# Optimization experiments

Hardware: AMD Instinct MI355X
Metric: run time of the kernel (lower is better)

Reference implementation:

```python
import jax, jax.numpy as jnp
import numpy as np
from jax import lax

BATCH = 512
FS = 24        # filter_size
QDIM = 11      # sort-of-clevr question vector length
IMG = 80       # 80 -> 40 -> 20 -> 10 -> 5 via four stride-2 convs
D = 5
OBJ = D * D    # 25 objects
PAIR_IN = (FS + 2) * 2 + QDIM  # 63
HID = 256
EPS = 1e-5


def setup_inputs() -> dict:
    key = jax.random.key(0)
    ks = jax.random.split(key, 24)

    def n(k, shape, s=0.05):
        return jax.random.normal(k, shape, jnp.float32) * s

    inp = {
        "img": jax.random.normal(ks[0], (BATCH, 3, IMG, IMG), jnp.float32),
        "qst": jax.random.normal(ks[1], (QDIM, BATCH), jnp.float32),
    }
    chans = [3, FS, FS, FS]
    ki = 2
    for l in range(4):
        inp[f"cw{l+1}"] = n(ks[ki], (FS, chans[l], 3, 3)); ki += 1
        inp[f"cb{l+1}"] = jnp.zeros((FS,), jnp.float32)
        inp[f"bg{l+1}"] = jnp.ones((FS,), jnp.float32)
        inp[f"bb{l+1}"] = jnp.zeros((FS,), jnp.float32)
    g_in = [PAIR_IN, HID, HID, HID]
    for l in range(4):
        inp[f"g{l+1}w"] = n(ks[ki], (HID, g_in[l])); ki += 1
        inp[f"g{l+1}b"] = jnp.zeros((HID,), jnp.float32)
    inp["f1w"] = n(ks[ki], (HID, HID)); ki += 1
    inp["f1b"] = jnp.zeros((HID,), jnp.float32)
    inp["fc2w"] = n(ks[ki], (HID, HID)); ki += 1
    inp["fc2b"] = jnp.zeros((HID,), jnp.float32)
    inp["fc3w"] = n(ks[ki], (10, HID)); ki += 1
    inp["fc3b"] = jnp.zeros((10,), jnp.float32)
    return inp


def _conv_bn(x, w, b, gamma, beta):
    # conv stride 2, pad 1 -> relu -> batchnorm (training-mode batch stats)
    y = lax.conv_general_dilated(x, w, (2, 2), [(1, 1), (1, 1)],
                                 dimension_numbers=("NCHW", "OIHW", "NCHW"))
    y = jax.nn.relu(y + b[None, :, None, None])
    mean = y.mean(axis=(0, 2, 3))
    var = y.var(axis=(0, 2, 3))
    inv = gamma * lax.rsqrt(var + EPS)
    return (y - mean[None, :, None, None]) * inv[None, :, None, None] + beta[None, :, None, None]


def _lin(x, w, b):
    return x @ w.T + b


def reference(img, qst,
              cw1, cb1, bg1, bb1, cw2, cb2, bg2, bb2,
              cw3, cb3, bg3, bb3, cw4, cb4, bg4, bb4,
              g1w, g1b, g2w, g2b, g3w, g3b, g4w, g4b,
              f1w, f1b, fc2w, fc2b, fc3w, fc3b):
    q = qst.T  # [mb, QDIM] (torch.transpose(qst,0,1).float())

    x = _conv_bn(img, cw1, cb1, bg1, bb1)
    x = _conv_bn(x, cw2, cb2, bg2, bb2)
    x = _conv_bn(x, cw3, cb3, bg3, bb3)
    x = _conv_bn(x, cw4, cb4, bg4, bb4)   # [mb, FS, 5, 5]

    mb = x.shape[0]
    x_flat = x.reshape(mb, FS, OBJ).transpose(0, 2, 1)  # [mb, 25, FS]

    idx = jnp.arange(OBJ)
    coord = jnp.stack([(idx // 5 - 2) / 2.0, (idx % 5 - 2) / 2.0], axis=-1).astype(jnp.float32)
    x_flat = jnp.concatenate([x_flat, jnp.broadcast_to(coord, (mb, OBJ, 2))], axis=2)  # [mb,25,FS+2]

    # pair[b, k, i] = concat(obj_i, obj_k, q)  (matches torch x_i/x_j/cat layout)
    oi = jnp.broadcast_to(x_flat[:, None, :, :], (mb, OBJ, OBJ, FS + 2))
    oj = jnp.broadcast_to(x_flat[:, :, None, :], (mb, OBJ, OBJ, FS + 2))
    qq = jnp.broadcast_to(q[:, None, None, :], (mb, OBJ, OBJ, QDIM))
    pairs = jnp.concatenate([oi, oj, qq], axis=3).reshape(mb * OBJ * OBJ, PAIR_IN)

    h = jax.nn.relu(_lin(pairs, g1w, g1b))
    h = jax.nn.relu(_lin(h, g2w, g2b))
    h = jax.nn.relu(_lin(h, g3w, g3b))
    h = jax.nn.relu(_lin(h, g4w, g4b))
    x_g = h.reshape(mb, OBJ * OBJ, HID).sum(axis=1)  # [mb, 256]

    x_f = jax.nn.relu(_lin(x_g, f1w, f1b))
    x_f = jax.nn.relu(_lin(x_f, fc2w, fc2b))
    # dropout treated as identity (eval-mode deterministic reference)
    logits = _lin(x_f, fc3w, fc3b)
    return jax.nn.log_softmax(logits, axis=-1)
```

## Files before the change

### kernel.cpp

```cpp
#include <hip/hip_runtime.h>
#include <math.h>

#define MB    512
#define FS    24
#define QDIM  11
#define OBJ   25
#define HID   256

typedef unsigned short u16;
typedef __attribute__((ext_vector_type(8))) __bf16 bf16x8;
typedef __attribute__((ext_vector_type(4))) __bf16 bf16x4;
typedef __attribute__((ext_vector_type(4))) float f32x4;
typedef __attribute__((ext_vector_type(8))) float f32x8;

__device__ __forceinline__ float bf2f(u16 h) {
    return __uint_as_float(((unsigned int)h) << 16);
}
__device__ __forceinline__ u16 f2bf(float f) {
    unsigned int u = __float_as_uint(f);
    return (u16)((u + 0x7FFFu + ((u >> 16) & 1u)) >> 16);
}

__global__ __launch_bounds__(256) void prep_all(
    const float* __restrict__ g2w, const float* __restrict__ g3w,
    const float* __restrict__ g4w, u16* __restrict__ wfrag,
    const float* __restrict__ cw1, const float* __restrict__ cw2,
    const float* __restrict__ cw3, const float* __restrict__ cw4,
    float* __restrict__ wt1, u16* __restrict__ wcfrag)
{
    if (blockIdx.x < 768) {
        int idx = blockIdx.x * 256 + threadIdx.x;
        int jj = idx & 7;
        int lane = (idx >> 3) & 63;
        int tn = (idx >> 9) & 15;
        int c = (idx >> 13) & 7;
        int l = idx >> 16;
        const float* W = (l == 0) ? g2w : ((l == 1) ? g3w : g4w);
        int n = tn * 16 + (lane & 15);
        int k = c * 32 + (lane >> 4) * 8 + jj;
        wfrag[idx] = f2bf(W[n * 256 + k]);
    } else {
        int idx = (blockIdx.x - 768) * 256 + threadIdx.x;
        if (idx < 648) {
            int k = idx / 24, oc = idx % 24;
            wt1[idx] = cw1[oc * 27 + k];
        } else if (idx < 648 + 27648) {
            int t = idx - 648;
            int l = t / 9216, r = t % 9216;
            int cell = r / 1024, rr = r % 1024;
            int o = rr / 512, q = rr % 512;
            int lane = q / 8, j = q % 8;
            int oc = o * 16 + (lane & 15);
            int ic = (lane >> 4) * 8 + j;
            const float* w = (l == 0) ? cw2 : ((l == 1) ? cw3 : cw4);
            u16 v = 0;
            if (oc < 24 && ic < 24) v = f2bf(w[oc * 216 + ic * 9 + cell]);
            wcfrag[t] = v;
        }
    }
}

__global__ __launch_bounds__(256) void conv1_t(
    const float* __restrict__ img, const float* __restrict__ wt1,
    const float* __restrict__ bias, float* __restrict__ yout,
    float* __restrict__ stats)
{
    __shared__ float tile[3 * 21 * 85];
    __shared__ float wS[648];
    __shared__ float part[48];
    const int tid = threadIdx.x;
    const int b   = blockIdx.x >> 2;
    const int y0  = (blockIdx.x & 3) * 10;
    const int iy_base = 2 * y0 - 1;
    for (int e = tid; e < 648; e += 256) wS[e] = wt1[e];
    for (int e = tid; e < 3 * 21 * 85; e += 256) {
        int ixt = e % 85; int rem = e / 85;
        int iyl = rem % 21; int ic = rem / 21;
        int iy = iy_base + iyl, ix = ixt - 1;
        float v = 0.f;
        if ((unsigned)iy < 80u && (unsigned)ix < 80u)
            v = img[((size_t)(b * 3 + ic) * 80 + iy) * 80 + ix];
        tile[e] = v;
    }
    if (tid < 48) part[tid] = 0.f;
    __syncthreads();

    float rsum[24], rsq[24];
#pragma unroll
    for (int oc = 0; oc < 24; oc++) { rsum[oc] = 0.f; rsq[oc] = 0.f; }

#pragma unroll 1
    for (int pp = 0; pp < 2; pp++) {
        const int pxl = tid + pp * 256;
        const bool active = pxl < 400;
        const int pxc = active ? pxl : 0;
        const int yl = pxc / 40, x = pxc % 40;
        float acc[24];
#pragma unroll
        for (int oc = 0; oc < 24; oc++) acc[oc] = bias[oc];
#pragma unroll 1
        for (int ic = 0; ic < 3; ic++) {
#pragma unroll 1
            for (int ky = 0; ky < 3; ky++) {
#pragma unroll 1
                for (int kx = 0; kx < 3; kx++) {
                    const int k = (ic * 3 + ky) * 3 + kx;
                    float xin = tile[ic * 1785 + (2 * yl + ky) * 85 + (2 * x + kx)];
                    const float4* wrow = (const float4*)&wS[k * 24];
#pragma unroll
                    for (int g = 0; g < 6; g++) {
                        float4 wv = wrow[g];
                        acc[g * 4 + 0] = fmaf(xin, wv.x, acc[g * 4 + 0]);
                        acc[g * 4 + 1] = fmaf(xin, wv.y, acc[g * 4 + 1]);
                        acc[g * 4 + 2] = fmaf(xin, wv.z, acc[g * 4 + 2]);
                        acc[g * 4 + 3] = fmaf(xin, wv.w, acc[g * 4 + 3]);
                    }
                }
            }
        }
#pragma unroll
        for (int oc = 0; oc < 24; oc++)
            acc[oc] = active ? fmaxf(acc[oc], 0.f) : 0.f;
        if (active) {
            float* op = &yout[((size_t)b * 1600 + (y0 + yl) * 40 + x) * 24];
#pragma unroll
            for (int g = 0; g < 6; g++)
                *(float4*)&op[g * 4] = make_float4(acc[g * 4], acc[g * 4 + 1],
                                                   acc[g * 4 + 2], acc[g * 4 + 3]);
        }
#pragma unroll
        for (int oc = 0; oc < 24; oc++) {
            rsum[oc] += acc[oc];
            rsq[oc]  += acc[oc] * acc[oc];
        }
    }

    {
        float v[48];
#pragma unroll
        for (int oc = 0; oc < 24; oc++) { v[oc] = rsum[oc]; v[24 + oc] = rsq[oc]; }
        const int ln = tid & 63;
#pragma unroll
        for (int i = 0; i < 48; i++) v[i] += __shfl_xor(v[i], 1, 64);
        {
            const bool bs = (ln & 1) != 0;
#pragma unroll
            for (int i = 0; i < 24; i++) v[i] = bs ? v[24 + i] : v[i];
        }
#pragma unroll
        for (int i = 0; i < 24; i++) v[i] += __shfl_xor(v[i], 2, 64);
        {
            const bool bs = (ln & 2) != 0;
#pragma unroll
            for (int i = 0; i < 12; i++) v[i] = bs ? v[12 + i] : v[i];
        }
#pragma unroll
        for (int i = 0; i < 12; i++) v[i] += __shfl_xor(v[i], 4, 64);
        {
            const bool bs = (ln & 4) != 0;
#pragma unroll
            for (int i = 0; i < 6; i++) v[i] = bs ? v[6 + i] : v[i];
        }
#pragma unroll
        for (int i = 0; i < 6; i++) v[i] += __shfl_xor(v[i], 8, 64);
        {
            const bool bs = (ln & 8) != 0;
#pragma unroll
            for (int i = 0; i < 3; i++) v[i] = bs ? v[3 + i] : v[i];
        }
#pragma unroll
        for (int i = 0; i < 3; i++) {
            v[i] += __shfl_xor(v[i], 16, 64);
            v[i] += __shfl_xor(v[i], 32, 64);
        }
        if (ln < 16) {
            const int base = (ln & 1) * 24 + ((ln >> 1) & 1) * 12
                           + ((ln >> 2) & 1) * 6 + ((ln >> 3) & 1) * 3;
#pragma unroll
            for (int i = 0; i < 3; i++) atomicAdd(&part[base + i], v[i]);
        }
    }
    __syncthreads();
    if (tid < 48) atomicAdd(&stats[tid], part[tid]);
}

template<int HIN, int HOUT, int YT, int MT>
__global__ __launch_bounds__(256) void convM(
    const float* __restrict__ yin,
    const float* __restrict__ stp, const float* __restrict__ gam,
    const float* __restrict__ bet, float invN,
    const u16* __restrict__ wcf_g,
    const float* __restrict__ bias,
    float* __restrict__ yout, float* __restrict__ stats)
{
    constexpr int ROWS = 2 * YT + 1;
    constexpr int R    = 2 * HOUT + 1;
    constexpr int POS  = ROWS * R;
    constexpr int NPX  = HOUT * HOUT;
    constexpr int NPXB = YT * HOUT;
    constexpr int TILES = HOUT / YT;
    constexpr int MTPW = (MT + 3) / 4;
    __shared__ __align__(16) u16 tile[POS * 24 + 16];
    __shared__ float scW[48];
    __shared__ float part[48];
    const int tid  = threadIdx.x;
    const int b    = (TILES == 1) ? blockIdx.x : (int)(blockIdx.x / TILES);
    const int y0   = (TILES == 1) ? 0 : (int)(blockIdx.x % TILES) * YT;
    const int lane = tid & 63, wave = tid >> 6;
    const int r16  = lane & 15, quad = lane >> 4;

    if (tid < 24) {
        float m   = stp[tid] * invN;
        float var = stp[24 + tid] * invN - m * m;
        float inv = gam[tid] * rsqrtf(var + 1e-5f);
        scW[tid]      = inv;
        scW[24 + tid] = bet[tid] - m * inv;
    }
    if (tid < 48) part[tid] = 0.f;

    bf16x8 wcf[9][2];
#pragma unroll
    for (int c = 0; c < 9; c++)
#pragma unroll
        for (int o = 0; o < 2; o++)
            wcf[c][o] = *(const bf16x8*)&wcf_g[((c * 2 + o) * 64 + lane) * 8];

    __syncthreads();

    f32x8 scv[3], ofv[3];
#pragma unroll
    for (int g = 0; g < 3; g++)
#pragma unroll
        for (int c2 = 0; c2 < 8; c2++) {
            scv[g][c2] = scW[g * 8 + c2];
            ofv[g][c2] = scW[24 + g * 8 + c2];
        }

    const int iy_base = 2 * y0 - 1;
    for (int p = tid; p < POS; p += 256) {
        int iyl = p / R, ixt = p % R;
        int iy = iy_base + iyl, ix = ixt - 1;
        if ((unsigned)iy < (unsigned)HIN && (unsigned)ix < (unsigned)HIN) {
            const float4* ip4 = (const float4*)&yin[((size_t)b * HIN * HIN + iy * HIN + ix) * 24];
#pragma unroll
            for (int g = 0; g < 3; g++) {
                float4 A = ip4[g * 2], B = ip4[g * 2 + 1];
                f32x8 xv = {A.x, A.y, A.z, A.w, B.x, B.y, B.z, B.w};
                f32x8 r = xv * scv[g] + ofv[g];
                bf16x8 hb = __builtin_convertvector(r, bf16x8);
                *(uint4*)&tile[p * 24 + g * 8] = *(uint4*)&hb;
            }
        } else {
            uint4 z = make_uint4(0, 0, 0, 0);
#pragma unroll
            for (int g = 0; g < 3; g++)
                *(uint4*)&tile[p * 24 + g * 8] = z;
        }
    }
    __syncthreads();

    f32x4 acc[MTPW][2];
#pragma unroll
    for (int t = 0; t < MTPW; t++) {
        acc[t][0] = (f32x4)(0.f);
        acc[t][1] = (f32x4)(0.f);
    }

    int baseT[MTPW];
#pragma unroll
    for (int t = 0; t < MTPW; t++) {
        int mt = wave + t * 4;
        int pxl = mt * 16 + r16;
        if (pxl > NPXB - 1) pxl = NPXB - 1;
        baseT[t] = ((2 * (pxl / HOUT)) * R + 2 * (pxl % HOUT)) * 24 + quad * 8;
    }

#pragma unroll
    for (int ky = 0; ky < 3; ky++) {
#pragma unroll
        for (int kx = 0; kx < 3; kx++) {
            const int cell = ky * 3 + kx;
            const int coff = (ky * R + kx) * 24;
            bf16x8 xf[MTPW];
#pragma unroll
            for (int t = 0; t < MTPW; t++) {
                int mt = wave + t * 4;
                uint4 tmp = make_uint4(0, 0, 0, 0);
                if (mt < MT && quad < 3)
                    tmp = *(const uint4*)&tile[baseT[t] + coff];
                xf[t] = *(bf16x8*)&tmp;
            }
#pragma unroll
            for (int t = 0; t < MTPW; t++) {
                int mt = wave + t * 4;
                if (mt < MT) {
                    acc[t][0] = __builtin_amdgcn_mfma_f32_16x16x32_bf16(
                        wcf[cell][0], xf[t], acc[t][0], 0, 0, 0);
                    acc[t][1] = __builtin_amdgcn_mfma_f32_16x16x32_bf16(
                        wcf[cell][1], xf[t], acc[t][1], 0, 0, 0);
                }
            }
        }
    }

    float ss[2][4], qq[2][4];
#pragma unroll
    for (int o = 0; o < 2; o++)
#pragma unroll
        for (int r = 0; r < 4; r++) { ss[o][r] = 0.f; qq[o][r] = 0.f; }

#pragma unroll
    for (int t = 0; t < MTPW; t++) {
        int mt = wave + t * 4;
        if (mt >= MT) continue;
        int pxl = mt * 16 + r16;
        bool pv = pxl < NPXB;
        int pxi = y0 * HOUT + pxl;
#pragma unroll
        for (int o = 0; o < 2; o++) {
            int ocb = o * 16 + quad * 4;
            if (pv && ocb < 24) {
                float4 bb = *(const float4*)&bias[ocb];
                float v0 = fmaxf(acc[t][o][0] + bb.x, 0.f);
                float v1 = fmaxf(acc[t][o][1] + bb.y, 0.f);
                float v2 = fmaxf(acc[t][o][2] + bb.z, 0.f);
                float v3 = fmaxf(acc[t][o][3] + bb.w, 0.f);
                *(float4*)&yout[((size_t)b * NPX + pxi) * 24 + ocb] =
                    make_float4(v0, v1, v2, v3);
                ss[o][0] += v0; qq[o][0] += v0 * v0;
                ss[o][1] += v1; qq[o][1] += v1 * v1;
                ss[o][2] += v2; qq[o][2] += v2 * v2;
                ss[o][3] += v3; qq[o][3] += v3 * v3;
            }
        }
    }
#pragma unroll
    for (int o = 0; o < 2; o++) {
        int ocb = o * 16 + quad * 4;
#pragma unroll
        for (int r = 0; r < 4; r++) {
            float a = ss[o][r], q = qq[o][r];
            a += __shfl_xor(a, 1, 64); q += __shfl_xor(q, 1, 64);
            a += __shfl_xor(a, 2, 64); q += __shfl_xor(q, 2, 64);
            a += __shfl_xor(a, 4, 64); q += __shfl_xor(q, 4, 64);
            a += __shfl_xor(a, 8, 64); q += __shfl_xor(q, 8, 64);
            if (r16 == 0 && ocb < 24) {
                atomicAdd(&part[ocb + r], a);
                atomicAdd(&part[24 + ocb + r], q);
            }
        }
    }
    __syncthreads();
    if (tid < 48) atomicAdd(&stats[tid], part[tid]);
}

__global__ __launch_bounds__(256) void uv_kernel(
    const float* __restrict__ y4t,
    const float* __restrict__ stp, const float* __restrict__ gam,
    const float* __restrict__ bet, float invN,
    const float* __restrict__ qst, const float* __restrict__ g1w,
    const float* __restrict__ g1b, u16* __restrict__ u, u16* __restrict__ v)
{
    int b = blockIdx.x, tid = threadIdx.x;
    __shared__ float xf[650];
    __shared__ float qv[11];
    __shared__ float scW[48];
    if (tid < 24) {
        float m   = stp[tid] * invN;
        float var = stp[24 + tid] * invN - m * m;
        float inv = gam[tid] * rsqrtf(var + 1e-5f);
        scW[tid]      = inv;
        scW[24 + tid] = bet[tid] - m * inv;
    }
    __syncthreads();
    for (int e = tid; e < 650; e += 256) {
        int o = e / 26, c = e % 26;
        float val;
        if (c < 24)      val = y4t[b * 600 + o * 24 + c] * scW[c] + scW[24 + c];
        else if (c == 24) val = (float)(o / 5 - 2) * 0.5f;
        else              val = (float)(o % 5 - 2) * 0.5f;
        xf[e] = val;
    }
    if (tid < 11) qv[tid] = qst[tid * MB + b];
    __syncthreads();
    const int n = tid;
    float wrow[63];
#pragma unroll
    for (int c = 0; c < 63; c++) wrow[c] = g1w[n * 63 + c];
    float qsum = g1b[n];
#pragma unroll
    for (int j = 0; j < 11; j++) qsum += wrow[52 + j] * qv[j];
    for (int o = 0; o < 25; o++) {
        float uu = 0.f, vv = qsum;
#pragma unroll
        for (int c = 0; c < 26; c++) {
            uu += wrow[c]      * xf[o * 26 + c];
            vv += wrow[26 + c] * xf[o * 26 + c];
        }
        u[(b * 25 + o) * 256 + n] = f2bf(uu);
        v[(b * 25 + o) * 256 + n] = f2bf(vv);
    }
}

__global__ __launch_bounds__(256, 2) void g_fused(
    const u16* __restrict__ u_bf, const u16* __restrict__ v_bf,
    const u16* __restrict__ wfrag,
    const float* __restrict__ b2, const float* __restrict__ b3, const float* __restrict__ b4,
    float* __restrict__ xg)
{
    __shared__ u16 hS[32768];
    const int tid  = threadIdx.x;
    const int b    = blockIdx.x / 5;
    const int p0   = (blockIdx.x % 5) * 128;
    const int lane = tid & 63, wave = tid >> 6;
    const int r16  = lane & 15, sub = lane >> 4;
    const int n0w  = wave * 64;

    const u16* wfL = wfrag + (size_t)(wave * 4) * 512 + (size_t)lane * 8;

    bf16x8 wcur[4], wnxt[4];
#pragma unroll
    for (int tn = 0; tn < 4; tn++)
        wcur[tn] = *(const bf16x8*)&wfL[(size_t)tn * 512];
#pragma unroll
    for (int tn = 0; tn < 4; tn++) wnxt[tn] = wcur[tn];

    {
        const int m = tid & 127, half = tid >> 7;
        const int p = p0 + m;
        if (p < 625) {
            const int oi = p % 25, ok = p / 25;
            const uint4* up = (const uint4*)(u_bf + (size_t)(b * 25 + oi) * 256);
            const uint4* vp = (const uint4*)(v_bf + (size_t)(b * 25 + ok) * 256);
#pragma unroll
            for (int gi = 0; gi < 16; gi++) {
                const int g = half * 16 + gi;
                uint4 ua = up[g], va = vp[g];
                bf16x8 ub = *(bf16x8*)&ua;
                bf16x8 vb = *(bf16x8*)&va;
                f32x8 uf = __builtin_convertvector(ub, f32x8);
                f32x8 vf = __builtin_convertvector(vb, f32x8);
                f32x8 hf = uf + vf;
                hf = __builtin_elementwise_max(hf, (f32x8)(0.f));
                bf16x8 hb = __builtin_convertvector(hf, bf16x8);
                *(uint4*)&hS[m * 256 + ((g ^ (m & 7)) * 8)] = *(uint4*)&hb;
            }
        } else {
            uint4 z = make_uint4(0, 0, 0, 0);
#pragma unroll
            for (int gi = 0; gi < 16; gi++) {
                const int g = half * 16 + gi;
                *(uint4*)&hS[m * 256 + ((g ^ (m & 7)) * 8)] = z;
            }
        }
    }

#pragma unroll 1
    for (int l = 0; l < 3; l++) {
        f32x4 acc[8][4];
#pragma unroll
        for (int tm = 0; tm < 8; tm++)
#pragma unroll
            for (int tn = 0; tn < 4; tn++)
                acc[tm][tn] = (f32x4)(0.f);

        __syncthreads();

#pragma unroll 1
        for (int kb = 0; kb < 8; kb++) {
            const int s = l * 8 + kb;
            if (s < 23) {
#pragma unroll
                for (int tn = 0; tn < 4; tn++)
                    wnxt[tn] = *(const bf16x8*)&wfL[((size_t)(s + 1) * 16 + tn) * 512];
            }
            bf16x8 bfr[8];
            const int g = kb * 4 + sub;
#pragma unroll
            for (int tm = 0; tm < 8; tm++) {
                const int m = tm * 16 + r16;
                bfr[tm] = *(const bf16x8*)&hS[m * 256 + ((g ^ (m & 7)) * 8)];
            }
#pragma unroll
            for (int tm = 0; tm < 8; tm++)
#pragma unroll
                for (int tn = 0; tn < 4; tn++)
                    acc[tm][tn] = __builtin_amdgcn_mfma_f32_16x16x32_bf16(
                        wcur[tn], bfr[tm], acc[tm][tn], 0, 0, 0);
#pragma unroll
            for (int tn = 0; tn < 4; tn++) wcur[tn] = wnxt[tn];
        }
        __syncthreads();

        const float* bl = (l == 0) ? b2 : ((l == 1) ? b3 : b4);
        if (l < 2) {
#pragma unroll
            for (int tn = 0; tn < 4; tn++) {
                const int n0 = n0w + tn * 16 + sub * 4;
                const float4 bb = *(const float4*)&bl[n0];
                const f32x4 bb4 = {bb.x, bb.y, bb.z, bb.w};
                const int gg = n0 >> 3;
                const int sh = (sub & 1) * 4;
#pragma unroll
                for (int tm = 0; tm < 8; tm++) {
                    const int m = tm * 16 + r16;
                    f32x4 t = acc[tm][tn] + bb4;
                    t = __builtin_elementwise_max(t, (f32x4)(0.f));
                    bf16x4 hb = __builtin_convertvector(t, bf16x4);
                    *(ushort4*)&hS[m * 256 + ((gg ^ (m & 7)) * 8) + sh] = *(ushort4*)&hb;
                }
            }
        } else {
            f32x4 sv[4];
#pragma unroll
            for (int tn = 0; tn < 4; tn++) sv[tn] = (f32x4)(0.f);
#pragma unroll
            for (int tn = 0; tn < 4; tn++) {
                const int n0 = n0w + tn * 16 + sub * 4;
                const float4 bb = *(const float4*)&bl[n0];
                const f32x4 bb4 = {bb.x, bb.y, bb.z, bb.w};
#pragma unroll
                for (int tm = 0; tm < 8; tm++) {
                    const int m = tm * 16 + r16;
                    if (p0 + m < 625) {
                        f32x4 t = acc[tm][tn] + bb4;
                        t = __builtin_elementwise_max(t, (f32x4)(0.f));
                        sv[tn] += t;
                    }
                }
            }
#pragma unroll
            for (int tn = 0; tn < 4; tn++)
#pragma unroll
                for (int r = 0; r < 4; r++) {
                    float v = sv[tn][r];
                    v += __shfl_xor(v, 1, 64);
                    v += __shfl_xor(v, 2, 64);
                    v += __shfl_xor(v, 4, 64);
                    v += __shfl_xor(v, 8, 64);
                    if (r16 == 0)
                        atomicAdd(&xg[b * 256 + n0w + tn * 16 + sub * 4 + r], v);
                }
        }
    }
}

__global__ __launch_bounds__(256) void f_fused(
    const float* __restrict__ xg,
    const float* __restrict__ f1w, const float* __restrict__ f1b,
    const float* __restrict__ fc2w, const float* __restrict__ fc2b,
    const float* __restrict__ fc3w, const float* __restrict__ fc3b,
    float* __restrict__ out)
{
    const int b = blockIdx.x, tid = threadIdx.x;
    __shared__ float xa[256], xb[256], lg[10], red[2];
    xa[tid] = xg[b * 256 + tid];
    __syncthreads();
    {
        const float4* wr = (const float4*)(f1w + (size_t)tid * 256);
        float a = f1b[tid];
#pragma unroll
        for (int k4 = 0; k4 < 64; k4++) {
            float4 w4 = wr[k4];
            a += w4.x * xa[k4 * 4 + 0] + w4.y * xa[k4 * 4 + 1]
               + w4.z * xa[k4 * 4 + 2] + w4.w * xa[k4 * 4 + 3];
        }
        xb[tid] = a > 0.f ? a : 0.f;
    }
    __syncthreads();
    {
        const float4* wr = (const float4*)(fc2w + (size_t)tid * 256);
        float a = fc2b[tid];
#pragma unroll
        for (int k4 = 0; k4 < 64; k4++) {
            float4 w4 = wr[k4];
            a += w4.x * xb[k4 * 4 + 0] + w4.y * xb[k4 * 4 + 1]
               + w4.z * xb[k4 * 4 + 2] + w4.w * xb[k4 * 4 + 3];
        }
        __syncthreads();
        xa[tid] = a > 0.f ? a : 0.f;
    }
    __syncthreads();
    if (tid < 10) {
        const float4* wr = (const float4*)(fc3w + (size_t)tid * 256);
        float a = fc3b[tid];
#pragma unroll
        for (int k4 = 0; k4 < 64; k4++) {
            float4 w4 = wr[k4];
            a += w4.x * xa[k4 * 4 + 0] + w4.y * xa[k4 * 4 + 1]
               + w4.z * xa[k4 * 4 + 2] + w4.w * xa[k4 * 4 + 3];
        }
        lg[tid] = a;
    }
    __syncthreads();
    if (tid == 0) {
        float mx = lg[0];
        for (int o = 1; o < 10; o++) mx = lg[o] > mx ? lg[o] : mx;
        float ssum = 0.f;
        for (int o = 0; o < 10; o++) ssum += expf(lg[o] - mx);
        red[0] = mx;
        red[1] = logf(ssum);
    }
    __syncthreads();
    if (tid < 10) out[b * 10 + tid] = lg[tid] - red[0] - red[1];
}

extern "C" void kernel_launch(void* const* d_in, const int* in_sizes, int n_in,
                              void* d_out, int out_size, void* d_ws, size_t ws_size,
                              hipStream_t stream)
{
    const float* img  = (const float*)d_in[0];
    const float* qst  = (const float*)d_in[1];
    const float* cw1  = (const float*)d_in[2];
    const float* cb1  = (const float*)d_in[3];
    const float* bg1  = (const float*)d_in[4];
    const float* bb1  = (const float*)d_in[5];
    const float* cw2  = (const float*)d_in[6];
    const float* cb2  = (const float*)d_in[7];
    const float* bg2  = (const float*)d_in[8];
    const float* bb2  = (const float*)d_in[9];
    const float* cw3  = (const float*)d_in[10];
    const float* cb3  = (const float*)d_in[11];
    const float* bg3  = (const float*)d_in[12];
    const float* bb3  = (const float*)d_in[13];
    const float* cw4  = (const float*)d_in[14];
    const float* cb4  = (const float*)d_in[15];
    const float* bg4  = (const float*)d_in[16];
    const float* bb4  = (const float*)d_in[17];
    const float* g1w  = (const float*)d_in[18];
    const float* g1b  = (const float*)d_in[19];
    const float* g2w  = (const float*)d_in[20];
    const float* g2b  = (const float*)d_in[21];
    const float* g3w  = (const float*)d_in[22];
    const float* g3b  = (const float*)d_in[23];
    const float* g4w  = (const float*)d_in[24];
    const float* g4b  = (const float*)d_in[25];
    const float* f1w  = (const float*)d_in[26];
    const float* f1b  = (const float*)d_in[27];
    const float* fc2w = (const float*)d_in[28];
    const float* fc2b = (const float*)d_in[29];
    const float* fc3w = (const float*)d_in[30];
    const float* fc3b = (const float*)d_in[31];
    float* out = (float*)d_out;

    float* ws    = (float*)d_ws;
    float* stats = ws;
    float* xg    = ws + 192;
    u16*   wfrag = (u16*)(ws + 131456);
    float* y1    = ws + 328064;
    float* y2    = ws + 19988864;
    float* y3    = ws + 24904064;
    float* y4    = ws + 26132864;
    u16*   u_bf  = (u16*)(ws + 26440064);
    u16*   v_bf  = (u16*)(ws + 28078464);
    float* wt1   = ws + 29716864;
    u16*   wcfrag = (u16*)(ws + 29717512);

    hipMemsetAsync(stats, 0, (size_t)131264 * sizeof(float), stream);

    prep_all<<<879, 256, 0, stream>>>(g2w, g3w, g4w, wfrag,
                                      cw1, cw2, cw3, cw4, wt1, wcfrag);

    conv1_t<<<2048, 256, 0, stream>>>(img, wt1, cb1, y1, stats);

    convM<40, 20, 4, 5><<<2560, 256, 0, stream>>>(
        y1, stats, bg1, bb1, 1.f / 819200.f, wcfrag, cb2, y2, stats + 48);
    convM<20, 10, 10, 7><<<512, 256, 0, stream>>>(
        y2, stats + 48, bg2, bb2, 1.f / 204800.f, wcfrag + 9216, cb3, y3, stats + 96);
    convM<10, 5, 5, 2><<<512, 256, 0, stream>>>(
        y3, stats + 96, bg3, bb3, 1.f / 51200.f, wcfrag + 18432, cb4, y4, stats + 144);

    uv_kernel<<<512, 256, 0, stream>>>(y4, stats + 144, bg4, bb4, 1.f / 12800.f,
                                       qst, g1w, g1b, u_bf, v_bf);

    g_fused<<<2560, 256, 0, stream>>>(u_bf, v_bf, wfrag, g2b, g3b, g4b, xg);

    f_fused<<<512, 256, 0, stream>>>(xg, f1w, f1b, fc2w, fc2b, fc3w, fc3b, out);
}
```

Before: 465.0 us.

## Split g_fused tile across 8 waves and drop weight register prefetch

The g_fused block grows from 256 to 512 threads, so eight waves split the 128-row tile into two row groups of four 16-row subtiles each, and each wave keeps half the accumulators. The software double-buffered weight prefetch (wcur/wnxt) is removed and weights are loaded per k-step instead. s_setprio is raised around the MFMA bursts. The aim is more waves in flight and fewer registers per wave to hide LDS and global latency, at the cost of weight fragments being read twice per block (once per row group) and load latency now being exposed inside each k-step.

```diff
diff --git a/kernel.cpp b/kernel.cpp
--- a/kernel.cpp
+++ b/kernel.cpp
@@ -402,7 +402,7 @@
     }
 }
 
-__global__ __launch_bounds__(256, 2) void g_fused(
+__global__ __launch_bounds__(512, 4) void g_fused(
     const u16* __restrict__ u_bf, const u16* __restrict__ v_bf,
     const u16* __restrict__ wfrag,
     const float* __restrict__ b2, const float* __restrict__ b3, const float* __restrict__ b4,
@@ -414,27 +414,22 @@
     const int p0   = (blockIdx.x % 5) * 128;
     const int lane = tid & 63, wave = tid >> 6;
     const int r16  = lane & 15, sub = lane >> 4;
-    const int n0w  = wave * 64;
-
-    const u16* wfL = wfrag + (size_t)(wave * 4) * 512 + (size_t)lane * 8;
-
-    bf16x8 wcur[4], wnxt[4];
-#pragma unroll
-    for (int tn = 0; tn < 4; tn++)
-        wcur[tn] = *(const bf16x8*)&wfL[(size_t)tn * 512];
-#pragma unroll
-    for (int tn = 0; tn < 4; tn++) wnxt[tn] = wcur[tn];
+    const int mgrp = wave >> 2;
+    const int ngrp = wave & 3;
+    const int n0w  = ngrp * 64;
+
+    const u16* wfL = wfrag + (size_t)(ngrp * 4) * 512 + (size_t)lane * 8;
 
     {
-        const int m = tid & 127, half = tid >> 7;
+        const int m = tid >> 2, q = tid & 3;
         const int p = p0 + m;
         if (p < 625) {
             const int oi = p % 25, ok = p / 25;
             const uint4* up = (const uint4*)(u_bf + (size_t)(b * 25 + oi) * 256);
             const uint4* vp = (const uint4*)(v_bf + (size_t)(b * 25 + ok) * 256);
 #pragma unroll
-            for (int gi = 0; gi < 16; gi++) {
-                const int g = half * 16 + gi;
+            for (int gi = 0; gi < 8; gi++) {
+                const int g = q * 8 + gi;
                 uint4 ua = up[g], va = vp[g];
                 bf16x8 ub = *(bf16x8*)&ua;
                 bf16x8 vb = *(bf16x8*)&va;
@@ -448,8 +443,8 @@
         } else {
             uint4 z = make_uint4(0, 0, 0, 0);
 #pragma unroll
-            for (int gi = 0; gi < 16; gi++) {
-                const int g = half * 16 + gi;
+            for (int gi = 0; gi < 8; gi++) {
+                const int g = q * 8 + gi;
                 *(uint4*)&hS[m * 256 + ((g ^ (m & 7)) * 8)] = z;
             }
         }
@@ -457,9 +452,9 @@
 
 #pragma unroll 1
     for (int l = 0; l < 3; l++) {
-        f32x4 acc[8][4];
-#pragma unroll
-        for (int tm = 0; tm < 8; tm++)
+        f32x4 acc[4][4];
+#pragma unroll
+        for (int tm = 0; tm < 4; tm++)
 #pragma unroll
             for (int tn = 0; tn < 4; tn++)
                 acc[tm][tn] = (f32x4)(0.f);
@@ -469,26 +464,25 @@
 #pragma unroll 1
         for (int kb = 0; kb < 8; kb++) {
             const int s = l * 8 + kb;
-            if (s < 23) {
-#pragma unroll
-                for (int tn = 0; tn < 4; tn++)
-                    wnxt[tn] = *(const bf16x8*)&wfL[((size_t)(s + 1) * 16 + tn) * 512];
-            }
-            bf16x8 bfr[8];
+            bf16x8 w[4];
+#pragma unroll
+            for (int tn = 0; tn < 4; tn++)
+                w[tn] = *(const bf16x8*)&wfL[((size_t)s * 16 + tn) * 512];
             const int g = kb * 4 + sub;
-#pragma unroll
-            for (int tm = 0; tm < 8; tm++) {
-                const int m = tm * 16 + r16;
+            bf16x8 bfr[4];
+#pragma unroll
+            for (int tm = 0; tm < 4; tm++) {
+                const int m = (mgrp * 4 + tm) * 16 + r16;
                 bfr[tm] = *(const bf16x8*)&hS[m * 256 + ((g ^ (m & 7)) * 8)];
             }
-#pragma unroll
-            for (int tm = 0; tm < 8; tm++)
+            __builtin_amdgcn_s_setprio(1);
+#pragma unroll
+            for (int tm = 0; tm < 4; tm++)
 #pragma unroll
                 for (int tn = 0; tn < 4; tn++)
                     acc[tm][tn] = __builtin_amdgcn_mfma_f32_16x16x32_bf16(
-                        wcur[tn], bfr[tm], acc[tm][tn], 0, 0, 0);
-#pragma unroll
-            for (int tn = 0; tn < 4; tn++) wcur[tn] = wnxt[tn];
+                        w[tn], bfr[tm], acc[tm][tn], 0, 0, 0);
+            __builtin_amdgcn_s_setprio(0);
         }
         __syncthreads();
 
@@ -502,8 +496,8 @@
                 const int gg = n0 >> 3;
                 const int sh = (sub & 1) * 4;
 #pragma unroll
-                for (int tm = 0; tm < 8; tm++) {
-                    const int m = tm * 16 + r16;
+                for (int tm = 0; tm < 4; tm++) {
+                    const int m = (mgrp * 4 + tm) * 16 + r16;
                     f32x4 t = acc[tm][tn] + bb4;
                     t = __builtin_elementwise_max(t, (f32x4)(0.f));
                     bf16x4 hb = __builtin_convertvector(t, bf16x4);
@@ -520,8 +514,8 @@
                 const float4 bb = *(const float4*)&bl[n0];
                 const f32x4 bb4 = {bb.x, bb.y, bb.z, bb.w};
 #pragma unroll
-                for (int tm = 0; tm < 8; tm++) {
-                    const int m = tm * 16 + r16;
+                for (int tm = 0; tm < 4; tm++) {
+                    const int m = (mgrp * 4 + tm) * 16 + r16;
                     if (p0 + m < 625) {
                         f32x4 t = acc[tm][tn] + bb4;
                         t = __builtin_elementwise_max(t, (f32x4)(0.f));
@@ -673,7 +667,7 @@
     uv_kernel<<<512, 256, 0, stream>>>(y4, stats + 144, bg4, bb4, 1.f / 12800.f,
                                        qst, g1w, g1b, u_bf, v_bf);
 
-    g_fused<<<2560, 256, 0, stream>>>(u_bf, v_bf, wfrag, g2b, g3b, g4b, xg);
+    g_fused<<<2560, 512, 0, stream>>>(u_bf, v_bf, wfrag, g2b, g3b, g4b, xg);
 
     f_fused<<<512, 256, 0, stream>>>(xg, f1w, f1b, fc2w, fc2b, fc3w, fc3b, out);
 }
```

After: 486.3 us. 4.6% more time.
